# Optimization experiments

Hardware: AMD Instinct MI355X
Metric: run time of the kernel (lower is better)

## Reference

```python
import jax, jax.numpy as jnp
import numpy as np

N_EMBED = 2048
NUM_EXPERTS = 64
TOP_K = 8
B, S = 4, 4096


def setup_inputs() -> dict:
    key = jax.random.key(0)
    k_x, k_n, k_w1, k_b1, k_w2, k_b2 = jax.random.split(key, 6)
    bound = 1.0 / np.sqrt(N_EMBED)  # torch nn.Linear default init range
    return {
        "x": jax.random.normal(k_x, (B, S, N_EMBED), dtype=jnp.float32),
        "noise": jax.random.normal(k_n, (B, S, NUM_EXPERTS), dtype=jnp.float32),
        "W1": jax.random.uniform(k_w1, (N_EMBED, NUM_EXPERTS), jnp.float32, -bound, bound),
        "b1": jax.random.uniform(k_b1, (NUM_EXPERTS,), jnp.float32, -bound, bound),
        "W2": jax.random.uniform(k_w2, (N_EMBED, NUM_EXPERTS), jnp.float32, -bound, bound),
        "b2": jax.random.uniform(k_b2, (NUM_EXPERTS,), jnp.float32, -bound, bound),
    }


def reference(x, noise, W1, b1, W2, b2):
    # logits = lin1(x); noise_scale = softplus(lin2(x))
    logits = jnp.einsum("bsd,de->bse", x, W1) + b1          # [B,S,E]
    scale = jax.nn.softplus(jnp.einsum("bsd,de->bse", x, W2) + b2)
    mixed = logits + noise * scale                            # [B,S,E]
    full = jax.nn.softmax(mixed, axis=-1)

    topk_vals, topk_idx = jax.lax.top_k(mixed, TOP_K)         # [B,S,K]

    # scatter topk values into a -inf background, then softmax (masked softmax)
    E = mixed.shape[-1]
    flat_mixed = mixed.reshape(-1, E)
    flat_idx = topk_idx.reshape(-1, TOP_K)
    flat_vals = topk_vals.reshape(-1, TOP_K)
    rows = jnp.arange(flat_mixed.shape[0])[:, None]
    sparse = jnp.full_like(flat_mixed, -jnp.inf).at[rows, flat_idx].set(flat_vals)
    sparse_sm = jax.nn.softmax(sparse, axis=-1).reshape(mixed.shape)

    return sparse_sm, topk_idx, full
```

## Files before the change

kernel.cpp:

```cpp
#include <hip/hip_runtime.h>
#include <math.h>


typedef _Float16 f16x8 __attribute__((ext_vector_type(8)));
typedef _Float16 f16x4 __attribute__((ext_vector_type(4)));
typedef float f32x4 __attribute__((ext_vector_type(4)));

constexpr int ND = 2048, NE = 64, NK = 8, NTOK = 16384;
constexpr int KC   = 32;
constexpr int NCHT = ND / KC;
constexpr int CPSG = 4;
constexpr int NSTG = NCHT / CPSG;
constexpr int HSTG = NSTG / 2;
constexpr int MTOK = 32;
constexpr int ZROW = 132;
constexpr int STG_F16 = CPSG * MTOK * 64;

__global__ void prep_w(const float* __restrict__ W1, const float* __restrict__ W2,
                       _Float16* __restrict__ wt3) {
    const int g    = blockIdx.x * 256 + threadIdx.x;
    const int cg   = g >> 9;
    const int rem  = g & 511;
    const int t    = rem >> 6;
    const int lane = rem & 63;
    const int col  = lane & 15, q = lane >> 4;
    const int n    = t * 16 + col;
    const float* W = (t < 4) ? W1 : W2;
    const int cn   = n & 63;
    _Float16 h[8], l[8];
    #pragma unroll
    for (int j = 0; j < 8; ++j) {
        const float v = W[(size_t)(cg * 32 + q * 8 + j) * 64 + cn];
        const _Float16 hh = (_Float16)v;
        h[j] = hh;
        l[j] = (_Float16)((v - (float)hh) * 2048.0f);
    }
    *(f16x8*)&wt3[((size_t)(cg * 2 + 0) * 8 + t) * 512 + lane * 8] = *(f16x8*)h;
    *(f16x8*)&wt3[((size_t)(cg * 2 + 1) * 8 + t) * 512 + lane * 8] = *(f16x8*)l;
}

__device__ __forceinline__ void split4(const float4 v, f16x4& hh, f16x4& ll) {
    const _Float16 h0 = (_Float16)v.x, h1 = (_Float16)v.y,
                   h2 = (_Float16)v.z, h3 = (_Float16)v.w;
    hh = (f16x4){h0, h1, h2, h3};
    ll = (f16x4){(_Float16)((v.x - (float)h0) * 2048.0f),
                 (_Float16)((v.y - (float)h1) * 2048.0f),
                 (_Float16)((v.z - (float)h2) * 2048.0f),
                 (_Float16)((v.w - (float)h3) * 2048.0f)};
}

__global__ __launch_bounds__(256, 2)
void router_fused(const float* __restrict__ x, const _Float16* __restrict__ wt3,
                  const float* __restrict__ noise,
                  const float* __restrict__ b1, const float* __restrict__ b2,
                  float* __restrict__ out_sparse, float* __restrict__ out_idx,
                  float* __restrict__ out_full) {
    __shared__ __align__(16) _Float16 stage[2][STG_F16];
    const int tid  = threadIdx.x;
    const int lane = tid & 63;
    const int wu   = __builtin_amdgcn_readfirstlane(tid >> 6);
    const int col  = lane & 15, q = lane >> 4;
    const long tok0 = (long)blockIdx.x * MTOK;
    const int ta = 2 * wu, tb = 2 * wu + 1;

    const int stok = tid >> 3, lsub = tid & 7;
    const float* xs = x + (tok0 + stok) * (size_t)ND + lsub * 4;
    const int wS = lsub >> 1, wh = lsub & 1;

    const _Float16* wla = wt3 + (size_t)ta * 512 + (size_t)lane * 8;
    const _Float16* wlb = wt3 + (size_t)tb * 512 + (size_t)lane * 8;

    f32x4 a0[2][2], a1[2][2], zk0[2][2];
    #pragma unroll
    for (int m = 0; m < 2; ++m)
        #pragma unroll
        for (int i = 0; i < 2; ++i)
            #pragma unroll
            for (int r = 0; r < 4; ++r) { a0[m][i][r] = 0.f; a1[m][i][r] = 0.f; }

    {
        float4 cur[4];
        #pragma unroll
        for (int j = 0; j < 4; ++j) cur[j] = *(const float4*)(xs + (size_t)j * KC);
        #pragma unroll
        for (int j = 0; j < 4; ++j) {
            f16x4 hv, lv; split4(cur[j], hv, lv);
            const int idx = ((j * MTOK + stok) << 6)
                          + (((wS ^ (stok & 7) ^ ((j & 1) << 2)) << 3) + (wh << 2));
            *(f16x4*)&stage[0][idx]      = hv;
            *(f16x4*)&stage[0][idx ^ 32] = lv;
        }
    }
    __syncthreads();

    for (int s = 0; s < NSTG; ++s) {
        const _Float16* rb = stage[s & 1];
        float4 nxt[4];
        if (s + 1 < NSTG) {
            #pragma unroll
            for (int j = 0; j < 4; ++j)
                nxt[j] = *(const float4*)(xs + (size_t)(s + 1) * 128 + (size_t)j * KC);
        }
        #pragma unroll
        for (int cc = 0; cc < CPSG; ++cc) {
            const size_t cb = (size_t)(s * CPSG + cc) * 8192;
            const f16x8 bha = *(const f16x8*)(wla + cb);
            const f16x8 bhb = *(const f16x8*)(wlb + cb);
            const f16x8 blx = *(const f16x8*)(wla + cb + 4096);
            const f16x8 bly = *(const f16x8*)(wlb + cb + 4096);
            const int swz = (cc & 1) << 2;
            #pragma unroll
            for (int mt = 0; mt < 2; ++mt) {
                const int ridx = ((cc * MTOK + mt * 16 + col) << 6)
                               + ((q ^ (col & 7) ^ swz) << 3);
                const f16x8 ah = *(const f16x8*)&rb[ridx];
                const f16x8 al = *(const f16x8*)&rb[ridx ^ 32];
                a0[mt][0] = __builtin_amdgcn_mfma_f32_16x16x32_f16(ah, bha, a0[mt][0], 0, 0, 0);
                a0[mt][1] = __builtin_amdgcn_mfma_f32_16x16x32_f16(ah, bhb, a0[mt][1], 0, 0, 0);
                a1[mt][0] = __builtin_amdgcn_mfma_f32_16x16x32_f16(ah, blx, a1[mt][0], 0, 0, 0);
                a1[mt][1] = __builtin_amdgcn_mfma_f32_16x16x32_f16(ah, bly, a1[mt][1], 0, 0, 0);
                a1[mt][0] = __builtin_amdgcn_mfma_f32_16x16x32_f16(al, bha, a1[mt][0], 0, 0, 0);
                a1[mt][1] = __builtin_amdgcn_mfma_f32_16x16x32_f16(al, bhb, a1[mt][1], 0, 0, 0);
            }
        }
        if (s == HSTG - 1) {
            #pragma unroll
            for (int m = 0; m < 2; ++m)
                #pragma unroll
                for (int i = 0; i < 2; ++i) {
                    zk0[m][i] = a0[m][i] + a1[m][i] * 4.8828125e-4f;
                    #pragma unroll
                    for (int r = 0; r < 4; ++r) { a0[m][i][r] = 0.f; a1[m][i][r] = 0.f; }
                }
        }
        if (s + 1 < NSTG) {
            _Float16* wb = stage[(s + 1) & 1];
            #pragma unroll
            for (int j = 0; j < 4; ++j) {
                f16x4 hv, lv; split4(nxt[j], hv, lv);
                const int idx = ((j * MTOK + stok) << 6)
                              + (((wS ^ (stok & 7) ^ ((j & 1) << 2)) << 3) + (wh << 2));
                *(f16x4*)&wb[idx]      = hv;
                *(f16x4*)&wb[idx ^ 32] = lv;
            }
        }
        __syncthreads();
    }

    float* zs = (float*)&stage[0][0];
    #pragma unroll
    for (int m = 0; m < 2; ++m)
        #pragma unroll
        for (int i = 0; i < 2; ++i) {
            const int n = (ta + i) * 16 + col;
            #pragma unroll
            for (int r = 0; r < 4; ++r) {
                const float zk1 = a0[m][i][r] + a1[m][i][r] * 4.8828125e-4f;
                const float comb = (float)((double)zk0[m][i][r] + (double)zk1);
                zs[(m * 16 + q * 4 + r) * ZROW + n] = comb;
            }
        }
    __syncthreads();

    const float b1v = b1[lane];
    const float b2v = b2[lane];
    for (int tt = 0; tt < 8; ++tt) {
        const int lt = wu * 8 + tt;
        const long tok = tok0 + lt;
        const float z1 = zs[lt * ZROW + lane] + b1v;
        const float z2 = zs[lt * ZROW + 64 + lane] + b2v;
        const float sc = (float)log1p(exp((double)z2));
        const float nz = noise[tok * NE + lane];
        const float mixed = z1 + nz * sc;

        float vmax = mixed;
        for (int off = 32; off; off >>= 1) vmax = fmaxf(vmax, __shfl_xor(vmax, off));
        const float e = expf(mixed - vmax);
        float denom = e;
        for (int off = 32; off; off >>= 1) denom += __shfl_xor(denom, off);
        const float fullv = e / denom;

        float cur = mixed;
        int   sel = 0;
        float myidxf = 0.0f;
        #pragma unroll
        for (int r = 0; r < NK; ++r) {
            float bv = cur; int bi = lane;
            for (int off = 32; off; off >>= 1) {
                const float ov = __shfl_xor(bv, off);
                const int   oi = __shfl_xor(bi, off);
                if (ov > bv || (ov == bv && oi < bi)) { bv = ov; bi = oi; }
            }
            if (lane == r)  myidxf = (float)bi;
            if (lane == bi) { sel = 1; cur = -INFINITY; }
        }

        const float es = sel ? e : 0.0f;
        float dsum = es;
        for (int off = 32; off; off >>= 1) dsum += __shfl_xor(dsum, off);
        const float sparsev = sel ? (e / dsum) : 0.0f;

        out_full[tok * NE + lane]   = fullv;
        out_sparse[tok * NE + lane] = sparsev;
        if (lane < NK) out_idx[tok * NK + lane] = myidxf;
    }
}

extern "C" void kernel_launch(void* const* d_in, const int* in_sizes, int n_in,
                              void* d_out, int out_size, void* d_ws, size_t ws_size,
                              hipStream_t stream) {
    const float* x     = (const float*)d_in[0];
    const float* noise = (const float*)d_in[1];
    const float* W1    = (const float*)d_in[2];
    const float* b1    = (const float*)d_in[3];
    const float* W2    = (const float*)d_in[4];
    const float* b2    = (const float*)d_in[5];

    float* out_sparse = (float*)d_out;
    float* out_idx    = out_sparse + (size_t)NTOK * NE;
    float* out_full   = out_idx + (size_t)NTOK * NK;

    _Float16* wt3 = (_Float16*)d_ws;

    prep_w<<<128, 256, 0, stream>>>(W1, W2, wt3);
    router_fused<<<NTOK / MTOK, 256, 0, stream>>>(x, wt3, noise, b1, b2,
                                                  out_sparse, out_idx, out_full);
}
```

Before: 262.5 us.

## Prefetch x two stages ahead and batch weight loads per stage

Global loads of x are now issued two stages ahead into ping-pong register buffers, with the main loop unrolled by two so the buffers swap statically. All weight fragments for a stage are loaded up front before the MFMA loop, giving the memory system more loads in flight. The aim is to hide global load latency behind MFMA work. The cost is higher register pressure, which could reduce occupancy.

```diff
diff --git a/kernel.cpp b/kernel.cpp
--- a/kernel.cpp
+++ b/kernel.cpp
@@ -78,36 +78,37 @@
             #pragma unroll
             for (int r = 0; r < 4; ++r) { a0[m][i][r] = 0.f; a1[m][i][r] = 0.f; }
 
-    {
-        float4 cur[4];
-        #pragma unroll
-        for (int j = 0; j < 4; ++j) cur[j] = *(const float4*)(xs + (size_t)j * KC);
+    float4 xa[4], xb[4];
+
+    auto deposit = [&](_Float16* wb, const float4 (&xr)[4]) {
         #pragma unroll
         for (int j = 0; j < 4; ++j) {
-            f16x4 hv, lv; split4(cur[j], hv, lv);
+            f16x4 hv, lv; split4(xr[j], hv, lv);
             const int idx = ((j * MTOK + stok) << 6)
                           + (((wS ^ (stok & 7) ^ ((j & 1) << 2)) << 3) + (wh << 2));
-            *(f16x4*)&stage[0][idx]      = hv;
-            *(f16x4*)&stage[0][idx ^ 32] = lv;
-        }
-    }
-    __syncthreads();
-
-    for (int s = 0; s < NSTG; ++s) {
-        const _Float16* rb = stage[s & 1];
-        float4 nxt[4];
-        if (s + 1 < NSTG) {
-            #pragma unroll
-            for (int j = 0; j < 4; ++j)
-                nxt[j] = *(const float4*)(xs + (size_t)(s + 1) * 128 + (size_t)j * KC);
-        }
+            *(f16x4*)&wb[idx]      = hv;
+            *(f16x4*)&wb[idx ^ 32] = lv;
+        }
+    };
+
+    auto do_stage = [&](const int s, const _Float16* rb, _Float16* wb,
+                        const float4 (&xw)[4], float4 (&xl)[4]) {
+        f16x8 B[CPSG][4];
         #pragma unroll
         for (int cc = 0; cc < CPSG; ++cc) {
             const size_t cb = (size_t)(s * CPSG + cc) * 8192;
-            const f16x8 bha = *(const f16x8*)(wla + cb);
-            const f16x8 bhb = *(const f16x8*)(wlb + cb);
-            const f16x8 blx = *(const f16x8*)(wla + cb + 4096);
-            const f16x8 bly = *(const f16x8*)(wlb + cb + 4096);
+            B[cc][0] = *(const f16x8*)(wla + cb);
+            B[cc][1] = *(const f16x8*)(wlb + cb);
+            B[cc][2] = *(const f16x8*)(wla + cb + 4096);
+            B[cc][3] = *(const f16x8*)(wlb + cb + 4096);
+        }
+        if (s + 2 < NSTG) {
+            #pragma unroll
+            for (int j = 0; j < 4; ++j)
+                xl[j] = *(const float4*)(xs + (size_t)(s + 2) * 128 + (size_t)j * KC);
+        }
+        #pragma unroll
+        for (int cc = 0; cc < CPSG; ++cc) {
             const int swz = (cc & 1) << 2;
             #pragma unroll
             for (int mt = 0; mt < 2; ++mt) {
@@ -115,12 +116,12 @@
                                + ((q ^ (col & 7) ^ swz) << 3);
                 const f16x8 ah = *(const f16x8*)&rb[ridx];
                 const f16x8 al = *(const f16x8*)&rb[ridx ^ 32];
-                a0[mt][0] = __builtin_amdgcn_mfma_f32_16x16x32_f16(ah, bha, a0[mt][0], 0, 0, 0);
-                a0[mt][1] = __builtin_amdgcn_mfma_f32_16x16x32_f16(ah, bhb, a0[mt][1], 0, 0, 0);
-                a1[mt][0] = __builtin_amdgcn_mfma_f32_16x16x32_f16(ah, blx, a1[mt][0], 0, 0, 0);
-                a1[mt][1] = __builtin_amdgcn_mfma_f32_16x16x32_f16(ah, bly, a1[mt][1], 0, 0, 0);
-                a1[mt][0] = __builtin_amdgcn_mfma_f32_16x16x32_f16(al, bha, a1[mt][0], 0, 0, 0);
-                a1[mt][1] = __builtin_amdgcn_mfma_f32_16x16x32_f16(al, bhb, a1[mt][1], 0, 0, 0);
+                a0[mt][0] = __builtin_amdgcn_mfma_f32_16x16x32_f16(ah, B[cc][0], a0[mt][0], 0, 0, 0);
+                a0[mt][1] = __builtin_amdgcn_mfma_f32_16x16x32_f16(ah, B[cc][1], a0[mt][1], 0, 0, 0);
+                a1[mt][0] = __builtin_amdgcn_mfma_f32_16x16x32_f16(ah, B[cc][2], a1[mt][0], 0, 0, 0);
+                a1[mt][1] = __builtin_amdgcn_mfma_f32_16x16x32_f16(ah, B[cc][3], a1[mt][1], 0, 0, 0);
+                a1[mt][0] = __builtin_amdgcn_mfma_f32_16x16x32_f16(al, B[cc][0], a1[mt][0], 0, 0, 0);
+                a1[mt][1] = __builtin_amdgcn_mfma_f32_16x16x32_f16(al, B[cc][1], a1[mt][1], 0, 0, 0);
             }
         }
         if (s == HSTG - 1) {
@@ -133,18 +134,24 @@
                     for (int r = 0; r < 4; ++r) { a0[m][i][r] = 0.f; a1[m][i][r] = 0.f; }
                 }
         }
-        if (s + 1 < NSTG) {
-            _Float16* wb = stage[(s + 1) & 1];
-            #pragma unroll
-            for (int j = 0; j < 4; ++j) {
-                f16x4 hv, lv; split4(nxt[j], hv, lv);
-                const int idx = ((j * MTOK + stok) << 6)
-                              + (((wS ^ (stok & 7) ^ ((j & 1) << 2)) << 3) + (wh << 2));
-                *(f16x4*)&wb[idx]      = hv;
-                *(f16x4*)&wb[idx ^ 32] = lv;
-            }
-        }
+        if (s + 1 < NSTG) deposit(wb, xw);
         __syncthreads();
+    };
+
+    {
+        float4 x0[4];
+        #pragma unroll
+        for (int j = 0; j < 4; ++j) x0[j] = *(const float4*)(xs + (size_t)j * KC);
+        deposit(stage[0], x0);
+        #pragma unroll
+        for (int j = 0; j < 4; ++j)
+            xa[j] = *(const float4*)(xs + (size_t)128 + (size_t)j * KC);
+    }
+    __syncthreads();
+
+    for (int sp = 0; sp < NSTG; sp += 2) {
+        do_stage(sp,     stage[0], stage[1], xa, xb);
+        do_stage(sp + 1, stage[1], stage[0], xb, xa);
     }
 
     float* zs = (float*)&stage[0][0];
```

Measured after the change: 256.8 us. -2.2%, faster.
